# Kernel optimization log

Measured on AMD Instinct MI355X. Metric: run time of the kernel, lower is better.

Reference implementation:

```python
import jax, jax.numpy as jnp
import numpy as np
import math

V, D, H, FF, L, S, B = 32000, 1024, 16, 4096, 8, 1024, 4
HD = D // H


def _pos_encoding(seq_len, dim):
    pos = np.arange(seq_len)[:, None].astype(np.float32)
    div = np.exp(np.arange(0, dim, 2).astype(np.float32) * -(math.log(10000.0) / dim))
    pe = np.zeros((seq_len, dim), dtype=np.float32)
    pe[:, 0::2] = np.sin(pos * div)
    pe[:, 1::2] = np.cos(pos * div)
    return jnp.asarray(pe)


def setup_inputs() -> dict:
    key = jax.random.key(0)
    ks = jax.random.split(key, 24)
    sc = 0.02
    inp = {
        'tokens': jax.random.randint(ks[0], (B, S), 0, V),
        'emb_W': jax.random.normal(ks[1], (V, D), jnp.float32) * sc,
        'Wq': jax.random.normal(ks[2], (L, D, D), jnp.float32) * sc,
        'bq': jnp.zeros((L, D), jnp.float32),
        'Wk': jax.random.normal(ks[3], (L, D, D), jnp.float32) * sc,
        'bk': jnp.zeros((L, D), jnp.float32),
        'Wv': jax.random.normal(ks[4], (L, D, D), jnp.float32) * sc,
        'bv': jnp.zeros((L, D), jnp.float32),
        'Wo': jax.random.normal(ks[5], (L, D, D), jnp.float32) * sc,
        'bo': jnp.zeros((L, D), jnp.float32),
        'ln1_g': jnp.ones((L, D), jnp.float32),
        'ln1_b': jnp.zeros((L, D), jnp.float32),
        'ln2_g': jnp.ones((L, D), jnp.float32),
        'ln2_b': jnp.zeros((L, D), jnp.float32),
        'W1': jax.random.normal(ks[6], (L, D, FF), jnp.float32) * sc,
        'b1': jnp.zeros((L, FF), jnp.float32),
        'W2': jax.random.normal(ks[7], (L, FF, D), jnp.float32) * sc,
        'b2': jnp.zeros((L, D), jnp.float32),
        'lnf_g': jnp.ones((D,), jnp.float32),
        'lnf_b': jnp.zeros((D,), jnp.float32),
        'head_W': jax.random.normal(ks[8], (D, V), jnp.float32) * sc,
        'head_b': jnp.zeros((V,), jnp.float32),
    }
    return inp


def _layernorm(x, g, b, eps=1e-5):
    mu = jnp.mean(x, axis=-1, keepdims=True)
    var = jnp.mean(jnp.square(x - mu), axis=-1, keepdims=True)
    return (x - mu) * jax.lax.rsqrt(var + eps) * g + b


def _attention(x, Wq, bq, Wk, bk, Wv, bv, Wo, bo, causal_mask):
    b, s, d = x.shape
    q = (x @ Wq + bq).reshape(b, s, H, HD).transpose(0, 2, 1, 3)
    k = (x @ Wk + bk).reshape(b, s, H, HD).transpose(0, 2, 1, 3)
    v = (x @ Wv + bv).reshape(b, s, H, HD).transpose(0, 2, 1, 3)
    scores = jnp.einsum('bhqd,bhkd->bhqk', q, k) / math.sqrt(HD)
    scores = jnp.where(causal_mask, scores, -1e9)
    attn = jax.nn.softmax(scores, axis=-1)
    out = jnp.einsum('bhqk,bhkd->bhqd', attn, v)
    out = out.transpose(0, 2, 1, 3).reshape(b, s, d)
    return out @ Wo + bo


def reference(tokens, emb_W, Wq, bq, Wk, bk, Wv, bv, Wo, bo,
              ln1_g, ln1_b, ln2_g, ln2_b, W1, b1, W2, b2,
              lnf_g, lnf_b, head_W, head_b):
    b, s = tokens.shape
    mask = jnp.tril(jnp.ones((s, s), bool))[None, None]  # (1,1,s,s)
    x = emb_W[tokens] + _pos_encoding(s, D)[None]
    for l in range(L):
        a = _attention(_layernorm(x, ln1_g[l], ln1_b[l]),
                       Wq[l], bq[l], Wk[l], bk[l], Wv[l], bv[l], Wo[l], bo[l], mask)
        x = x + a
        h = _layernorm(x, ln2_g[l], ln2_b[l])
        h = jax.nn.relu(h @ W1[l] + b1[l]) @ W2[l] + b2[l]
        x = x + h
    x = _layernorm(x, lnf_g, lnf_b)
    return x @ head_W + head_b
```

## Files before the change

### kernel.cpp

```cpp
#include <hip/hip_runtime.h>
#include <math.h>


using u16 = unsigned short;
using u32 = unsigned int;
typedef __attribute__((ext_vector_type(4))) float  f32x4;
typedef __attribute__((ext_vector_type(8))) short  s16x8;
typedef __attribute__((ext_vector_type(8))) __bf16 bf16x8;

__device__ __forceinline__ u16 f2bf(float f) {
  u32 u = __builtin_bit_cast(u32, f);
  u += 0x7fffu + ((u >> 16) & 1u);
  return (u16)(u >> 16);
}

__device__ __forceinline__ f32x4 mfma16(s16x8 a, s16x8 b, f32x4 c) {
  return __builtin_amdgcn_mfma_f32_16x16x32_bf16(
      __builtin_bit_cast(bf16x8, a), __builtin_bit_cast(bf16x8, b), c, 0, 0, 0);
}

#define GLD16(gp, lp) __builtin_amdgcn_global_load_lds(                    \
    (const __attribute__((address_space(1))) void*)(gp),                   \
    (__attribute__((address_space(3))) void*)(lp), 16, 0, 0)

__global__ __launch_bounds__(256) void transpose_cvt(
    const float* __restrict__ in, u16* __restrict__ out,
    int C, long long inLS, long long outLS, int outRS)
{
  __shared__ float t[32][33];
  int tr = threadIdx.x >> 5, tc = threadIdx.x & 31;
  const float* ip = in + (size_t)blockIdx.z * inLS +
                    ((size_t)blockIdx.x * 32 + tr) * C + blockIdx.y * 32 + tc;
#pragma unroll
  for (int p = 0; p < 4; ++p) t[p * 8 + tr][tc] = ip[(size_t)p * 8 * C];
  __syncthreads();
  u16* op = out + (size_t)blockIdx.z * outLS +
            ((size_t)blockIdx.y * 32 + tr) * outRS + (size_t)blockIdx.x * 32 + tc;
#pragma unroll
  for (int p = 0; p < 4; ++p) op[(size_t)p * 8 * outRS] = f2bf(t[tc][p * 8 + tr]);
}

__global__ __launch_bounds__(256) void pack_bqkv(
    const float* __restrict__ bq, const float* __restrict__ bk,
    const float* __restrict__ bv, float* __restrict__ outb)
{
  int i = blockIdx.x * 256 + threadIdx.x;
  int ly = i / 3072, j = i % 3072;
  float v = (j < 1024) ? bq[ly * 1024 + j]
          : (j < 2048) ? bk[ly * 1024 + (j - 1024)]
                       : bv[ly * 1024 + (j - 2048)];
  outb[i] = v;
}

__global__ __launch_bounds__(256) void embed_kernel(
    const int* __restrict__ tokens, const float* __restrict__ embW,
    float* __restrict__ x)
{
  int row = blockIdx.x;
  int s = row & 1023;
  int tok = tokens[row];
  int d0 = threadIdx.x * 4;
  float4 e = *(const float4*)&embW[(size_t)tok * 1024 + d0];
  const float c = -9.210340371976184f / 1024.0f;
  float div0 = expf((float)d0 * c);
  float div1 = expf((float)(d0 + 2) * c);
  float sn0, cs0, sn1, cs1;
  sincosf((float)s * div0, &sn0, &cs0);
  sincosf((float)s * div1, &sn1, &cs1);
  float4 r;
  r.x = e.x + sn0; r.y = e.y + cs0; r.z = e.z + sn1; r.w = e.w + cs1;
  *(float4*)&x[(size_t)row * 1024 + d0] = r;
}

__global__ __launch_bounds__(256) void ln_kernel(
    const float* __restrict__ x, const float* __restrict__ g,
    const float* __restrict__ b, u16* __restrict__ y)
{
  int row = blockIdx.x, tid = threadIdx.x;
  float4 v = *(const float4*)&x[(size_t)row * 1024 + tid * 4];
  float sum = v.x + v.y + v.z + v.w;
  float sq = v.x * v.x + v.y * v.y + v.z * v.z + v.w * v.w;
#pragma unroll
  for (int o = 32; o > 0; o >>= 1) {
    sum += __shfl_xor(sum, o, 64);
    sq  += __shfl_xor(sq,  o, 64);
  }
  __shared__ float ps[8];
  int w = tid >> 6;
  if ((tid & 63) == 0) { ps[w] = sum; ps[4 + w] = sq; }
  __syncthreads();
  sum = ps[0] + ps[1] + ps[2] + ps[3];
  sq  = ps[4] + ps[5] + ps[6] + ps[7];
  float mu = sum * (1.0f / 1024.0f);
  float var = sq * (1.0f / 1024.0f) - mu * mu;
  float rs = rsqrtf(var + 1e-5f);
  float4 gg = *(const float4*)&g[tid * 4];
  float4 bb = *(const float4*)&b[tid * 4];
  u32 lo = (u32)f2bf((v.x - mu) * rs * gg.x + bb.x) |
           ((u32)f2bf((v.y - mu) * rs * gg.y + bb.y) << 16);
  u32 hi = (u32)f2bf((v.z - mu) * rs * gg.z + bb.z) |
           ((u32)f2bf((v.w - mu) * rs * gg.w + bb.w) << 16);
  uint2 o2; o2.x = lo; o2.y = hi;
  *(uint2*)&y[(size_t)row * 1024 + tid * 4] = o2;
}

template<int OMODE, int RELU>
__global__ __launch_bounds__(512, 2) void gemm256(
    const u16* __restrict__ A, const u16* __restrict__ Bt,
    const float* __restrict__ bias, void* Cp, int M, int N, int K, int gx)
{
  __shared__ alignas(16) u16 lds[4][16384];
  const int tid = threadIdx.x;
  const int w = tid >> 6, l = tid & 63;
  const int g = l >> 4, lr = l & 15;
  const int wm = w >> 2, wn = w & 3;
  int nwg = gridDim.x;
  int bid = blockIdx.x;
  int swz = (bid & 7) * (nwg >> 3) + (bid >> 3);
  int bx = swz % gx, by = swz / gx;
  int m0 = by << 8, n0 = bx << 8;

  const u16* Ag[2]; const u16* Bg[2]; int dstE[2];
#pragma unroll
  for (int s2 = 0; s2 < 2; ++s2) {
    int idx = s2 * 512 + tid;
    int row = idx >> 2;
    int ch = (idx & 3) ^ ((row >> 1) & 3);
    Ag[s2] = A  + (size_t)(m0 + row) * K + ch * 8;
    Bg[s2] = Bt + (size_t)(n0 + row) * K + ch * 8;
    dstE[s2] = idx * 8;
  }
  const int colx = (g ^ ((lr >> 1) & 3)) * 8;
  const int aoff = (wm * 128 + lr) * 32 + colx;
  const int boff = 8192 + (wn * 64 + lr) * 32 + colx;

  f32x4 acc[8][4];
#pragma unroll
  for (int i = 0; i < 8; ++i)
#pragma unroll
    for (int j = 0; j < 4; ++j) acc[i][j] = f32x4{0.f, 0.f, 0.f, 0.f};

  const int nk = K >> 5;
#pragma unroll
  for (int pt = 0; pt < 3; ++pt) {
    u16* buf = &lds[pt][0];
#pragma unroll
    for (int s2 = 0; s2 < 2; ++s2) GLD16(Ag[s2] + pt * 32, buf + dstE[s2]);
#pragma unroll
    for (int s2 = 0; s2 < 2; ++s2) GLD16(Bg[s2] + pt * 32, buf + 8192 + dstE[s2]);
  }
  asm volatile("s_waitcnt vmcnt(8)" ::: "memory");
  __builtin_amdgcn_s_barrier();

  u16* p0 = &lds[0][0];
  u16* p1 = &lds[1][0];
  u16* p2 = &lds[2][0];
  u16* p3 = &lds[3][0];

  s16x8 aC[4], bC[4];
#pragma unroll
  for (int i = 0; i < 4; ++i) aC[i] = *(const s16x8*)&p0[aoff + i * 512];
#pragma unroll
  for (int j = 0; j < 4; ++j) bC[j] = *(const s16x8*)&p0[boff + j * 512];

  for (int t = 0; t < nk; ++t) {
    const int rem = nk - 1 - t;
    s16x8 aH[4];
#pragma unroll
    for (int i = 0; i < 4; ++i) aH[i] = *(const s16x8*)&p0[aoff + (4 + i) * 512];
    if (rem >= 3) {
      const int k3 = t * 32 + 96;
#pragma unroll
      for (int s2 = 0; s2 < 2; ++s2) GLD16(Ag[s2] + k3, p3 + dstE[s2]);
#pragma unroll
      for (int s2 = 0; s2 < 2; ++s2) GLD16(Bg[s2] + k3, p3 + 8192 + dstE[s2]);
    }
    __builtin_amdgcn_s_setprio(1);
#pragma unroll
    for (int i = 0; i < 4; ++i)
#pragma unroll
      for (int j = 0; j < 4; ++j) acc[i][j] = mfma16(aC[i], bC[j], acc[i][j]);
    __builtin_amdgcn_s_setprio(0);
    if (rem >= 3)      asm volatile("s_waitcnt vmcnt(8)" ::: "memory");
    else if (rem == 2) asm volatile("s_waitcnt vmcnt(4)" ::: "memory");
    else if (rem == 1) asm volatile("s_waitcnt vmcnt(0)" ::: "memory");
    __builtin_amdgcn_s_barrier();
    s16x8 aN[4], bN[4];
    if (rem >= 1) {
#pragma unroll
      for (int i = 0; i < 4; ++i) aN[i] = *(const s16x8*)&p1[aoff + i * 512];
#pragma unroll
      for (int j = 0; j < 4; ++j) bN[j] = *(const s16x8*)&p1[boff + j * 512];
    }
    __builtin_amdgcn_s_setprio(1);
#pragma unroll
    for (int i = 0; i < 4; ++i)
#pragma unroll
      for (int j = 0; j < 4; ++j) acc[4 + i][j] = mfma16(aH[i], bC[j], acc[4 + i][j]);
    __builtin_amdgcn_s_setprio(0);
    __builtin_amdgcn_s_barrier();
    u16* tmp = p0; p0 = p1; p1 = p2; p2 = p3; p3 = tmp;
#pragma unroll
    for (int i = 0; i < 4; ++i) { aC[i] = aN[i]; bC[i] = bN[i]; }
  }

  float* fst = (float*)(void*)&lds[0][0];
#pragma unroll
  for (int mf = 0; mf < 8; ++mf) {
    __builtin_amdgcn_s_barrier();
#pragma unroll
    for (int nf = 0; nf < 4; ++nf) {
      int cl = wn * 64 + nf * 16 + lr;
      float bv = bias[n0 + cl];
      int rl = wm * 16 + g * 4;
#pragma unroll
      for (int r = 0; r < 4; ++r) {
        float v = acc[mf][nf][r] + bv;
        if (RELU) v = fmaxf(v, 0.f);
        fst[(rl + r) * 260 + cl] = v;
      }
    }
    __builtin_amdgcn_s_barrier();
    if (OMODE == 0) {
#pragma unroll
      for (int it = 0; it < 2; ++it) {
        int seg = it * 512 + tid;
        int row = seg >> 5;
        int co  = (seg & 31) * 8;
        int grow = m0 + (row >> 4) * 128 + mf * 16 + (row & 15);
        const float* src = &fst[row * 260 + co];
        uint4 q;
        q.x = (u32)f2bf(src[0]) | ((u32)f2bf(src[1]) << 16);
        q.y = (u32)f2bf(src[2]) | ((u32)f2bf(src[3]) << 16);
        q.z = (u32)f2bf(src[4]) | ((u32)f2bf(src[5]) << 16);
        q.w = (u32)f2bf(src[6]) | ((u32)f2bf(src[7]) << 16);
        *(uint4*)&((u16*)Cp)[(size_t)grow * N + n0 + co] = q;
      }
    } else {
#pragma unroll
      for (int it = 0; it < 4; ++it) {
        int seg = it * 512 + tid;
        int row = seg >> 6;
        int co  = (seg & 63) * 4;
        int grow = m0 + (row >> 4) * 128 + mf * 16 + (row & 15);
        float4 q = *(float4*)&fst[row * 260 + co];
        *(float4*)&((float*)Cp)[(size_t)grow * N + n0 + co] = q;
      }
    }
  }
}

template<int OMODE, int RELU>
__global__ __launch_bounds__(256, 3) void gemm_p(
    const u16* __restrict__ A, const u16* __restrict__ Bt,
    const float* __restrict__ bias, const float* res, void* Cp,
    int M, int N, int K, int gx)
{
  __shared__ alignas(16) u16 lds[2][8192];
  const int tid = threadIdx.x;
  const int w = tid >> 6, l = tid & 63;
  const int g = l >> 4, lr = l & 15;
  const int wm = w >> 1, wn = w & 1;
  int nwg = gridDim.x;
  int bid = blockIdx.x;
  int swz = (bid & 7) * (nwg >> 3) + (bid >> 3);
  int bx = swz % gx, by = swz / gx;
  int m0 = by << 7, n0 = bx << 7;

  const u16 *Ag[2], *Bg[2];
  int dstA[2], dstB[2];
#pragma unroll
  for (int s = 0; s < 2; ++s) {
    int idx = s * 256 + tid;
    int row = idx >> 2;
    int ch = (idx & 3) ^ ((row >> 1) & 3);
    Ag[s] = A  + (size_t)(m0 + row) * K + ch * 8;
    Bg[s] = Bt + (size_t)(n0 + row) * K + ch * 8;
    dstA[s] = idx * 8;
    dstB[s] = 4096 + idx * 8;
  }
  const int colx = (g ^ ((lr >> 1) & 3)) * 8;
  const int aoff = (wm * 64 + lr) * 32 + colx;
  const int boff = 4096 + (wn * 64 + lr) * 32 + colx;

  f32x4 acc[4][4];
#pragma unroll
  for (int i = 0; i < 4; ++i)
#pragma unroll
    for (int j = 0; j < 4; ++j) acc[i][j] = f32x4{0.f, 0.f, 0.f, 0.f};

  const int nk = K >> 5;
#pragma unroll
  for (int s = 0; s < 2; ++s) GLD16(Ag[s], &lds[0][dstA[s]]);
#pragma unroll
  for (int s = 0; s < 2; ++s) GLD16(Bg[s], &lds[0][dstB[s]]);
  asm volatile("s_waitcnt vmcnt(0)" ::: "memory");
  __builtin_amdgcn_s_barrier();

  int cur = 0;
  s16x8 aC[4], bC[4];
#pragma unroll
  for (int i = 0; i < 4; ++i) aC[i] = *(const s16x8*)&lds[0][aoff + i * 512];
#pragma unroll
  for (int j = 0; j < 4; ++j) bC[j] = *(const s16x8*)&lds[0][boff + j * 512];

  for (int t = 0; t < nk; ++t) {
    const bool more = (t + 1 < nk);
    if (more) {
      const int kn = (t + 1) << 5;
#pragma unroll
      for (int s = 0; s < 2; ++s) GLD16(Ag[s] + kn, &lds[cur ^ 1][dstA[s]]);
#pragma unroll
      for (int s = 0; s < 2; ++s) GLD16(Bg[s] + kn, &lds[cur ^ 1][dstB[s]]);
    }
    __builtin_amdgcn_s_setprio(1);
#pragma unroll
    for (int i = 0; i < 4; ++i)
#pragma unroll
      for (int j = 0; j < 4; ++j) acc[i][j] = mfma16(aC[i], bC[j], acc[i][j]);
    __builtin_amdgcn_s_setprio(0);
    if (more) {
      asm volatile("s_waitcnt vmcnt(0)" ::: "memory");
      __builtin_amdgcn_s_barrier();
      cur ^= 1;
#pragma unroll
      for (int i = 0; i < 4; ++i) aC[i] = *(const s16x8*)&lds[cur][aoff + i * 512];
#pragma unroll
      for (int j = 0; j < 4; ++j) bC[j] = *(const s16x8*)&lds[cur][boff + j * 512];
    }
  }
#pragma unroll
  for (int mf = 0; mf < 4; ++mf) {
    int row = m0 + wm * 64 + mf * 16 + g * 4;
#pragma unroll
    for (int nf = 0; nf < 4; ++nf) {
      int col = n0 + wn * 64 + nf * 16 + lr;
      float bv = bias[col];
#pragma unroll
      for (int r = 0; r < 4; ++r) {
        float v = acc[mf][nf][r] + bv;
        if (RELU) v = fmaxf(v, 0.f);
        size_t idx = (size_t)(row + r) * N + col;
        if (OMODE == 0)      ((u16*)Cp)[idx] = f2bf(v);
        else if (OMODE == 1) ((float*)Cp)[idx] = v + res[idx];
        else                 ((float*)Cp)[idx] = v;
      }
    }
  }
}

__global__ __launch_bounds__(256) void attn_kernel(
    const u16* __restrict__ qkv, u16* __restrict__ outp)
{
  int b = blockIdx.x >> 4, h = blockIdx.x & 15;
  int q0 = blockIdx.y << 6;
  int tid = threadIdx.x, w = tid >> 6, l = tid & 63;
  int g = l >> 4, lr = l & 15;
  const int RS = 3072;
  const u16* base = qkv + (size_t)b * 1024 * RS + h * 64;
  const u16* Qb = base;
  const u16* Kb = base + 1024;
  const u16* Vb = base + 2048;
  __shared__ alignas(16) u16 Plds[4][1024];
  __shared__ alignas(16) u16 Vt[4096];
  char* Pw = (char*)&Plds[w][0];

  s16x8 qf[2];
#pragma unroll
  for (int ks = 0; ks < 2; ++ks)
    qf[ks] = *(const s16x8*)&Qb[(size_t)(q0 + w * 16 + lr) * RS + ks * 32 + g * 8];

  f32x4 o[4];
#pragma unroll
  for (int n = 0; n < 4; ++n) o[n] = f32x4{0.f, 0.f, 0.f, 0.f};
  float mr[4] = {-INFINITY, -INFINITY, -INFINITY, -INFINITY};
  float ls[4] = {0.f, 0.f, 0.f, 0.f};

  int ntile = (q0 >> 6) + 1;
  for (int kt = 0; kt < ntile; ++kt) {
    int kv0 = kt << 6;
    f32x4 sc[4];
#pragma unroll
    for (int t = 0; t < 4; ++t) sc[t] = f32x4{0.f, 0.f, 0.f, 0.f};
#pragma unroll
    for (int ks = 0; ks < 2; ++ks)
#pragma unroll
      for (int t = 0; t < 4; ++t) {
        s16x8 kf = *(const s16x8*)&Kb[(size_t)(kv0 + t * 16 + lr) * RS + ks * 32 + g * 8];
        sc[t] = mfma16(qf[ks], kf, sc[t]);
      }
#pragma unroll
    for (int p = 0; p < 2; ++p) {
      int key = p * 32 + (tid >> 3);
      int d0 = (tid & 7) * 8;
      s16x8 vrow = *(const s16x8*)&Vb[(size_t)(kv0 + key) * RS + d0];
#pragma unroll
      for (int j = 0; j < 8; ++j) {
        int d = d0 + j;
        int byt = (d * 128 + key * 2) ^ ((d & 7) << 4);
        *(u16*)((char*)Vt + byt) = (u16)vrow[j];
      }
    }
    float p4[4][4];
    float tmax[4] = {-INFINITY, -INFINITY, -INFINITY, -INFINITY};
    int qr_base = q0 + w * 16 + g * 4;
#pragma unroll
    for (int t = 0; t < 4; ++t) {
      int key = kv0 + t * 16 + lr;
#pragma unroll
      for (int r = 0; r < 4; ++r) {
        float s = sc[t][r] * 0.125f;
        s = (key <= qr_base + r) ? s : -1e30f;
        p4[t][r] = s;
        tmax[r] = fmaxf(tmax[r], s);
      }
    }
#pragma unroll
    for (int off = 1; off < 16; off <<= 1)
#pragma unroll
      for (int r = 0; r < 4; ++r) tmax[r] = fmaxf(tmax[r], __shfl_xor(tmax[r], off, 64));
    float corr[4], rsum[4];
#pragma unroll
    for (int r = 0; r < 4; ++r) {
      float mn = fmaxf(mr[r], tmax[r]);
      corr[r] = __expf(mr[r] - mn);
      mr[r] = mn;
      rsum[r] = 0.f;
    }
#pragma unroll
    for (int t = 0; t < 4; ++t)
#pragma unroll
      for (int r = 0; r < 4; ++r) {
        float e = __expf(p4[t][r] - mr[r]);
        p4[t][r] = e;
        rsum[r] += e;
      }
#pragma unroll
    for (int off = 1; off < 16; off <<= 1)
#pragma unroll
      for (int r = 0; r < 4; ++r) rsum[r] += __shfl_xor(rsum[r], off, 64);
#pragma unroll
    for (int r = 0; r < 4; ++r) ls[r] = ls[r] * corr[r] + rsum[r];
#pragma unroll
    for (int n = 0; n < 4; ++n)
#pragma unroll
      for (int r = 0; r < 4; ++r) o[n][r] *= corr[r];
#pragma unroll
    for (int t = 0; t < 4; ++t)
#pragma unroll
      for (int r = 0; r < 4; ++r) {
        int prow = g * 4 + r;
        int byt = (prow * 128 + (t * 16 + lr) * 2) ^ ((prow & 7) << 4);
        *(u16*)(Pw + byt) = f2bf(p4[t][r]);
      }
    __syncthreads();
#pragma unroll
    for (int ks = 0; ks < 2; ++ks) {
      int ab = (lr * 128 + ks * 64 + g * 16) ^ ((lr & 7) << 4);
      s16x8 pa = *(const s16x8*)(Pw + ab);
#pragma unroll
      for (int n = 0; n < 4; ++n) {
        int vb2 = ((n * 16 + lr) * 128 + ks * 64 + g * 16) ^ ((lr & 7) << 4);
        s16x8 vfr = *(const s16x8*)((const char*)Vt + vb2);
        o[n] = mfma16(pa, vfr, o[n]);
      }
    }
    __syncthreads();
  }
#pragma unroll
  for (int n = 0; n < 4; ++n)
#pragma unroll
    for (int r = 0; r < 4; ++r) {
      float v = o[n][r] / ls[r];
      outp[(size_t)(b * 1024 + q0 + w * 16 + g * 4 + r) * 1024 + h * 64 + n * 16 + lr] = f2bf(v);
    }
}

extern "C" void kernel_launch(void* const* d_in, const int* in_sizes, int n_in,
                              void* d_out, int out_size, void* d_ws, size_t ws_size,
                              hipStream_t stream)
{
  const int*   tokens = (const int*)  d_in[0];
  const float* embW   = (const float*)d_in[1];
  const float* Wq     = (const float*)d_in[2];
  const float* bq     = (const float*)d_in[3];
  const float* Wk     = (const float*)d_in[4];
  const float* bk     = (const float*)d_in[5];
  const float* Wv     = (const float*)d_in[6];
  const float* bv     = (const float*)d_in[7];
  const float* Wo     = (const float*)d_in[8];
  const float* bo     = (const float*)d_in[9];
  const float* ln1g   = (const float*)d_in[10];
  const float* ln1b   = (const float*)d_in[11];
  const float* ln2g   = (const float*)d_in[12];
  const float* ln2b   = (const float*)d_in[13];
  const float* W1     = (const float*)d_in[14];
  const float* b1     = (const float*)d_in[15];
  const float* W2     = (const float*)d_in[16];
  const float* b2     = (const float*)d_in[17];
  const float* lnfg   = (const float*)d_in[18];
  const float* lnfb   = (const float*)d_in[19];
  const float* headW  = (const float*)d_in[20];
  const float* headb  = (const float*)d_in[21];
  (void)in_sizes; (void)n_in; (void)out_size;

  char* ws = (char*)d_ws;
  u16*   qkvT = (u16*)(ws);
  u16*   woT  = (u16*)(ws + 50331648);
  u16*   w1T  = (u16*)(ws + 67108864);
  u16*   w2T  = (u16*)(ws + 134217728);
  u16*   headT= (u16*)(ws + 201326592);
  float* bqkv = (float*)(ws + 266862592);
  float* x    = (float*)(ws + 266960896);
  u16*   y    = (u16*)(ws + 283738112);
  u16*   qkv  = (u16*)(ws + 292126720);
  u16*   attno= (u16*)(ws + 317292544);
  u16*   h1   = (u16*)(ws + 325681152);
  if (ws_size < 359235584ull) return;

  dim3 blk(256);
  dim3 blk5(512);
  transpose_cvt<<<dim3(32, 32, 8),  blk, 0, stream>>>(Wq, qkvT,           1024,  1048576LL, 3145728LL, 1024);
  transpose_cvt<<<dim3(32, 32, 8),  blk, 0, stream>>>(Wk, qkvT + 1048576, 1024,  1048576LL, 3145728LL, 1024);
  transpose_cvt<<<dim3(32, 32, 8),  blk, 0, stream>>>(Wv, qkvT + 2097152, 1024,  1048576LL, 3145728LL, 1024);
  transpose_cvt<<<dim3(32, 32, 8),  blk, 0, stream>>>(Wo, woT,            1024,  1048576LL, 1048576LL, 1024);
  transpose_cvt<<<dim3(32, 128, 8), blk, 0, stream>>>(W1, w1T,            4096,  4194304LL, 4194304LL, 1024);
  transpose_cvt<<<dim3(128, 32, 8), blk, 0, stream>>>(W2, w2T,            1024,  4194304LL, 4194304LL, 4096);
  transpose_cvt<<<dim3(32, 1000, 1),blk, 0, stream>>>(headW, headT,       32000, 0LL,       0LL,       1024);
  pack_bqkv<<<96, blk, 0, stream>>>(bq, bk, bv, bqkv);
  embed_kernel<<<4096, blk, 0, stream>>>(tokens, embW, x);
  for (int ly = 0; ly < 8; ++ly) {
    ln_kernel<<<4096, blk, 0, stream>>>(x, ln1g + ly * 1024, ln1b + ly * 1024, y);
    gemm256<0, 0><<<192, blk5, 0, stream>>>(y, qkvT + (size_t)ly * 3145728,
        bqkv + ly * 3072, qkv, 4096, 3072, 1024, 12);
    attn_kernel<<<dim3(64, 16), blk, 0, stream>>>(qkv, attno);
    gemm_p<1, 0><<<256, blk, 0, stream>>>(attno, woT + (size_t)ly * 1048576,
        bo + ly * 1024, x, x, 4096, 1024, 1024, 8);
    ln_kernel<<<4096, blk, 0, stream>>>(x, ln2g + ly * 1024, ln2b + ly * 1024, y);
    gemm256<0, 1><<<256, blk5, 0, stream>>>(y, w1T + (size_t)ly * 4194304,
        b1 + ly * 4096, h1, 4096, 4096, 1024, 16);
    gemm_p<1, 0><<<256, blk, 0, stream>>>(h1, w2T + (size_t)ly * 4194304,
        b2 + ly * 1024, x, x, 4096, 1024, 4096, 8);
  }
  ln_kernel<<<4096, blk, 0, stream>>>(x, lnfg, lnfb, y);
  gemm256<2, 0><<<2000, blk5, 0, stream>>>(y, headT, headb,
      (float*)d_out, 4096, 32000, 1024, 125);
}
```

Before: 2.743 ms.

## Switch gemm256 to double-buffered LDS pipeline and nontemporal head output stores

Replaces the 4-stage LDS ring (three tiles in flight, split A-fragment reads between MFMA halves) with a simple 2-buffer scheme. It loads the next tile while computing the current one, then waits on vmcnt(0) and a barrier each iteration. LDS use halves from 128KB to 64KB per block, which may allow more blocks per CU, but it exposes more global-load latency per k-step. It also adds a template flag that uses nontemporal stores for the large fp32 logits output of the head GEMM.

```diff
diff --git a/kernel.cpp b/kernel.cpp
--- a/kernel.cpp
+++ b/kernel.cpp
@@ -104,12 +104,12 @@
   *(uint2*)&y[(size_t)row * 1024 + tid * 4] = o2;
 }
 
-template<int OMODE, int RELU>
+template<int OMODE, int RELU, int NT>
 __global__ __launch_bounds__(512, 2) void gemm256(
     const u16* __restrict__ A, const u16* __restrict__ Bt,
     const float* __restrict__ bias, void* Cp, int M, int N, int K, int gx)
 {
-  __shared__ alignas(16) u16 lds[4][16384];
+  __shared__ alignas(16) u16 lds[2][16384];
   const int tid = threadIdx.x;
   const int w = tid >> 6, l = tid & 63;
   const int g = l >> 4, lr = l & 15;
@@ -142,66 +142,51 @@
 
   const int nk = K >> 5;
 #pragma unroll
-  for (int pt = 0; pt < 3; ++pt) {
-    u16* buf = &lds[pt][0];
-#pragma unroll
-    for (int s2 = 0; s2 < 2; ++s2) GLD16(Ag[s2] + pt * 32, buf + dstE[s2]);
-#pragma unroll
-    for (int s2 = 0; s2 < 2; ++s2) GLD16(Bg[s2] + pt * 32, buf + 8192 + dstE[s2]);
-  }
-  asm volatile("s_waitcnt vmcnt(8)" ::: "memory");
+  for (int s2 = 0; s2 < 2; ++s2) GLD16(Ag[s2], &lds[0][dstE[s2]]);
+#pragma unroll
+  for (int s2 = 0; s2 < 2; ++s2) GLD16(Bg[s2], &lds[0][8192 + dstE[s2]]);
+  asm volatile("s_waitcnt vmcnt(0)" ::: "memory");
   __builtin_amdgcn_s_barrier();
 
-  u16* p0 = &lds[0][0];
-  u16* p1 = &lds[1][0];
-  u16* p2 = &lds[2][0];
-  u16* p3 = &lds[3][0];
-
-  s16x8 aC[4], bC[4];
-#pragma unroll
-  for (int i = 0; i < 4; ++i) aC[i] = *(const s16x8*)&p0[aoff + i * 512];
-#pragma unroll
-  for (int j = 0; j < 4; ++j) bC[j] = *(const s16x8*)&p0[boff + j * 512];
+  int cur = 0;
+  s16x8 aC[4], aH[4], bC[4];
+#pragma unroll
+  for (int i = 0; i < 4; ++i) aC[i] = *(const s16x8*)&lds[0][aoff + i * 512];
+#pragma unroll
+  for (int i = 0; i < 4; ++i) aH[i] = *(const s16x8*)&lds[0][aoff + (4 + i) * 512];
+#pragma unroll
+  for (int j = 0; j < 4; ++j) bC[j] = *(const s16x8*)&lds[0][boff + j * 512];
 
   for (int t = 0; t < nk; ++t) {
-    const int rem = nk - 1 - t;
-    s16x8 aH[4];
-#pragma unroll
-    for (int i = 0; i < 4; ++i) aH[i] = *(const s16x8*)&p0[aoff + (4 + i) * 512];
-    if (rem >= 3) {
-      const int k3 = t * 32 + 96;
-#pragma unroll
-      for (int s2 = 0; s2 < 2; ++s2) GLD16(Ag[s2] + k3, p3 + dstE[s2]);
-#pragma unroll
-      for (int s2 = 0; s2 < 2; ++s2) GLD16(Bg[s2] + k3, p3 + 8192 + dstE[s2]);
+    const bool more = (t + 1 < nk);
+    if (more) {
+      const int kn = (t + 1) << 5;
+#pragma unroll
+      for (int s2 = 0; s2 < 2; ++s2) GLD16(Ag[s2] + kn, &lds[cur ^ 1][dstE[s2]]);
+#pragma unroll
+      for (int s2 = 0; s2 < 2; ++s2) GLD16(Bg[s2] + kn, &lds[cur ^ 1][8192 + dstE[s2]]);
     }
     __builtin_amdgcn_s_setprio(1);
 #pragma unroll
     for (int i = 0; i < 4; ++i)
 #pragma unroll
       for (int j = 0; j < 4; ++j) acc[i][j] = mfma16(aC[i], bC[j], acc[i][j]);
-    __builtin_amdgcn_s_setprio(0);
-    if (rem >= 3)      asm volatile("s_waitcnt vmcnt(8)" ::: "memory");
-    else if (rem == 2) asm volatile("s_waitcnt vmcnt(4)" ::: "memory");
-    else if (rem == 1) asm volatile("s_waitcnt vmcnt(0)" ::: "memory");
-    __builtin_amdgcn_s_barrier();
-    s16x8 aN[4], bN[4];
-    if (rem >= 1) {
-#pragma unroll
-      for (int i = 0; i < 4; ++i) aN[i] = *(const s16x8*)&p1[aoff + i * 512];
-#pragma unroll
-      for (int j = 0; j < 4; ++j) bN[j] = *(const s16x8*)&p1[boff + j * 512];
-    }
-    __builtin_amdgcn_s_setprio(1);
 #pragma unroll
     for (int i = 0; i < 4; ++i)
 #pragma unroll
       for (int j = 0; j < 4; ++j) acc[4 + i][j] = mfma16(aH[i], bC[j], acc[4 + i][j]);
     __builtin_amdgcn_s_setprio(0);
-    __builtin_amdgcn_s_barrier();
-    u16* tmp = p0; p0 = p1; p1 = p2; p2 = p3; p3 = tmp;
-#pragma unroll
-    for (int i = 0; i < 4; ++i) { aC[i] = aN[i]; bC[i] = bN[i]; }
+    if (more) {
+      asm volatile("s_waitcnt vmcnt(0)" ::: "memory");
+      __builtin_amdgcn_s_barrier();
+      cur ^= 1;
+#pragma unroll
+      for (int i = 0; i < 4; ++i) aC[i] = *(const s16x8*)&lds[cur][aoff + i * 512];
+#pragma unroll
+      for (int i = 0; i < 4; ++i) aH[i] = *(const s16x8*)&lds[cur][aoff + (4 + i) * 512];
+#pragma unroll
+      for (int j = 0; j < 4; ++j) bC[j] = *(const s16x8*)&lds[cur][boff + j * 512];
+    }
   }
 
   float* fst = (float*)(void*)&lds[0][0];
@@ -243,8 +228,10 @@
         int row = seg >> 6;
         int co  = (seg & 63) * 4;
         int grow = m0 + (row >> 4) * 128 + mf * 16 + (row & 15);
-        float4 q = *(float4*)&fst[row * 260 + co];
-        *(float4*)&((float*)Cp)[(size_t)grow * N + n0 + co] = q;
+        f32x4 q = *(const f32x4*)&fst[row * 260 + co];
+        float* dp = &((float*)Cp)[(size_t)grow * N + n0 + co];
+        if (NT) __builtin_nontemporal_store(q, (f32x4*)dp);
+        else    *(f32x4*)dp = q;
       }
     }
   }
@@ -531,18 +518,18 @@
   embed_kernel<<<4096, blk, 0, stream>>>(tokens, embW, x);
   for (int ly = 0; ly < 8; ++ly) {
     ln_kernel<<<4096, blk, 0, stream>>>(x, ln1g + ly * 1024, ln1b + ly * 1024, y);
-    gemm256<0, 0><<<192, blk5, 0, stream>>>(y, qkvT + (size_t)ly * 3145728,
+    gemm256<0, 0, 0><<<192, blk5, 0, stream>>>(y, qkvT + (size_t)ly * 3145728,
         bqkv + ly * 3072, qkv, 4096, 3072, 1024, 12);
     attn_kernel<<<dim3(64, 16), blk, 0, stream>>>(qkv, attno);
     gemm_p<1, 0><<<256, blk, 0, stream>>>(attno, woT + (size_t)ly * 1048576,
         bo + ly * 1024, x, x, 4096, 1024, 1024, 8);
     ln_kernel<<<4096, blk, 0, stream>>>(x, ln2g + ly * 1024, ln2b + ly * 1024, y);
-    gemm256<0, 1><<<256, blk5, 0, stream>>>(y, w1T + (size_t)ly * 4194304,
+    gemm256<0, 1, 0><<<256, blk5, 0, stream>>>(y, w1T + (size_t)ly * 4194304,
         b1 + ly * 4096, h1, 4096, 4096, 1024, 16);
     gemm_p<1, 0><<<256, blk, 0, stream>>>(h1, w2T + (size_t)ly * 4194304,
         b2 + ly * 1024, x, x, 4096, 1024, 4096, 8);
   }
   ln_kernel<<<4096, blk, 0, stream>>>(x, lnfg, lnfb, y);
-  gemm256<2, 0><<<2000, blk5, 0, stream>>>(y, headT, headb,
+  gemm256<2, 0, 1><<<2000, blk5, 0, stream>>>(y, headT, headb,
       (float*)d_out, 4096, 32000, 1024, 125);
 }
```

New measurement: 2.776 ms. About the same (+1.2%).
